# Kernel optimization log

Hardware: AMD Instinct MI355X
Metric: run time of the kernel (lower is better)

The kernel has to match this reference:

```python
import jax, jax.numpy as jnp
import numpy as np

P = 512        # number of graph pairs
MAXN = 192     # max(len_s) by construction
D_IN = 32      # num_input_features
HID = 64       # hidden_dim
REG = 0.1      # entropic reg
ITERS = 8      # numItermax in forward call
DEG = 8        # avg degree for synthetic edges


def setup_inputs() -> dict:
    key = jax.random.key(0)
    ks = jax.random.split(key, 16)
    len_s = np.asarray(96 + (np.arange(P) % 97), dtype=np.int32)          # 96..192
    len_t = np.asarray(32 + ((np.arange(P) * 7) % 65), dtype=np.int32)    # 32..96 <= len_s
    Ns, Nt = int(len_s.sum()), int(len_t.sum())
    return {
        "x_s": jax.random.normal(ks[0], (Ns, D_IN), jnp.float32),
        "x_t": jax.random.normal(ks[1], (Nt, D_IN), jnp.float32),
        "W_rel0": 0.1 * jax.random.normal(ks[2], (D_IN, HID), jnp.float32),
        "b_rel0": 0.1 * jax.random.normal(ks[3], (HID,), jnp.float32),
        "W_root0": 0.1 * jax.random.normal(ks[4], (D_IN, HID), jnp.float32),
        "W_rel1": 0.1 * jax.random.normal(ks[5], (HID, HID), jnp.float32),
        "b_rel1": 0.1 * jax.random.normal(ks[6], (HID,), jnp.float32),
        "W_root1": 0.1 * jax.random.normal(ks[7], (HID, HID), jnp.float32),
        "W_e": 0.1 * jax.random.normal(ks[8], (D_IN + 2 * HID, 64), jnp.float32),
        "b_e": 0.1 * jax.random.normal(ks[9], (64,), jnp.float32),
        "virtual": jax.random.uniform(ks[10], (64,), jnp.float32),
        "edge_index_s": jax.random.randint(ks[11], (2, Ns * DEG), 0, Ns, dtype=jnp.int32),
        "edge_index_t": jax.random.randint(ks[12], (2, Nt * DEG), 0, Nt, dtype=jnp.int32),
        "len_s": jnp.asarray(len_s),
        "len_t": jnp.asarray(len_t),
    }


def _normalize(x):
    return x / jnp.clip(jnp.linalg.norm(x, axis=-1, keepdims=True), 1e-12)


def _gnn_embed(x, ei, layers, W_e, b_e):
    # GraphConv: out = lin_rel(sum_{j->i} x_j) + lin_root(x_i), then relu; cat all layer outputs
    outs = [x]
    h = x
    for (Wr, br, Wo) in layers:
        agg = jax.ops.segment_sum(h[ei[0]], ei[1], num_segments=h.shape[0])
        h = jax.nn.relu(agg @ Wr + br + h @ Wo)
        outs.append(h)
    emb = jnp.concatenate(outs, axis=1) @ W_e + b_e
    return _normalize(emb)


def _pad_gather(emb, lens):
    # [total, E] -> [P, MAXN, E] via per-pair offsets (indices clipped; invalid masked later)
    off = jnp.cumsum(lens) - lens
    idx = jnp.clip(off[:, None] + jnp.arange(MAXN)[None, :], 0, emb.shape[0] - 1)
    return emb[idx]


def reference(x_s, x_t, W_rel0, b_rel0, W_root0, W_rel1, b_rel1, W_root1,
              W_e, b_e, virtual, edge_index_s, edge_index_t, len_s, len_t):
    layers = [(W_rel0, b_rel0, W_root0), (W_rel1, b_rel1, W_root1)]
    emb_s = _gnn_embed(x_s, edge_index_s, layers, W_e, b_e)  # [Ns, 64]
    emb_t = _gnn_embed(x_t, edge_index_t, layers, W_e, b_e)  # [Nt, 64]
    virt = _normalize(virtual[None, :])[0]

    s_pad = _pad_gather(emb_s, len_s)  # [P, MAXN, 64]
    t_pad = _pad_gather(emb_t, len_t)  # [P, MAXN, 64]
    j = jnp.arange(MAXN)
    # columns >= len_t use the virtual node embedding (covers j in [m, n))
    t_mask = (j[None, :] < len_t[:, None])[:, :, None]
    t_aug = jnp.where(t_mask, t_pad, virt[None, None, :])

    # Euclidean cdist via quadratic expansion
    sq_s = jnp.sum(s_pad * s_pad, -1)                              # [P, MAXN]
    sq_t = jnp.sum(t_aug * t_aug, -1)                              # [P, MAXN]
    dot = jnp.einsum('pid,pjd->pij', s_pad, t_aug)                 # [P, MAXN, MAXN]
    cd = jnp.sqrt(jnp.maximum(sq_s[:, :, None] + sq_t[:, None, :] - 2.0 * dot, 1e-12))

    # padded cost: real block = cdist, bottom-right pad block = 0, rest = 1000
    row_valid = j[None, :] < len_s[:, None]                        # [P, MAXN] (n = len_s)
    in_block = row_valid[:, :, None] & row_valid[:, None, :]
    pad_block = (~row_valid)[:, :, None] & (~row_valid)[:, None, :]
    cost = jnp.where(in_block, cd, jnp.where(pad_block, 0.0, 1000.0))

    # Sinkhorn-Knopp, a = b = ones(MAXN) so Kp = K and updates are 1/(K v), 1/(K^T u)
    K = jnp.exp(-cost / REG)

    def body(_, uv):
        u, v = uv
        v = 1.0 / jnp.einsum('pij,pi->pj', K, u)
        u = 1.0 / jnp.einsum('pij,pj->pi', K, v)
        return (u, v)

    u0 = jnp.full((P, MAXN), 1.0 / MAXN, dtype=cost.dtype)
    u, v = jax.lax.fori_loop(0, ITERS, body, (u0, u0))
    gamma = jax.lax.stop_gradient(u[:, :, None] * K * v[:, None, :])

    geds = jnp.sum(gamma * cost, axis=(1, 2))
    geds2 = geds / (len_s + len_t).astype(cost.dtype)
    return gamma, cost, geds2
```

## Files before the change

kernel.cpp:

```cpp
#include <hip/hip_runtime.h>
#include <math.h>

#define PAIRS 512
#define MAXN 192

#define LDS_BAR() asm volatile("s_waitcnt lgkmcnt(0)\n\ts_barrier" ::: "memory")

__global__ void offsets_kernel(const int* __restrict__ ls, const int* __restrict__ lt,
                               int* __restrict__ off) {
    __shared__ int wa[8], wb[8];
    int t = threadIdx.x;
    int a = ls[t], b = lt[t];
    int ia = a, ib = b;
#pragma unroll
    for (int d = 1; d < 64; d <<= 1) {
        int xa = __shfl_up(ia, d, 64);
        int xb = __shfl_up(ib, d, 64);
        if ((t & 63) >= d) { ia += xa; ib += xb; }
    }
    if ((t & 63) == 63) { wa[t >> 6] = ia; wb[t >> 6] = ib; }
    __syncthreads();
    int pa = 0, pb = 0;
    for (int w = 0; w < (t >> 6); w++) { pa += wa[w]; pb += wb[w]; }
    off[t] = pa + ia - a;
    off[PAIRS + t] = pb + ib - b;
}

__global__ __launch_bounds__(256) void count2_kernel(const int* __restrict__ eiS,
                                                     const int* __restrict__ eiT,
                                                     int* __restrict__ cnt,
                                                     int Es, int Et, int split) {
    int e = blockIdx.x * 256 + threadIdx.x;
    if (e < Es) atomicAdd(&cnt[eiS[Es + e]], 1);
    else if (e < Es + Et) atomicAdd(&cnt[split + eiT[Et + (e - Es)]], 1);
}

__global__ __launch_bounds__(256) void scan1_kernel(int* __restrict__ data,
                                                    int* __restrict__ blockSums, int N) {
    __shared__ int sc[256];
    int t = threadIdx.x;
    int base = blockIdx.x * 1024;
    int v[4];
    int s = 0;
#pragma unroll
    for (int q = 0; q < 4; q++) {
        int i = base + t * 4 + q;
        v[q] = (i < N) ? data[i] : 0;
        s += v[q];
    }
    sc[t] = s;
    __syncthreads();
    for (int d = 1; d < 256; d <<= 1) {
        int x = (t >= d) ? sc[t - d] : 0;
        __syncthreads();
        sc[t] += x;
        __syncthreads();
    }
    int excl = sc[t] - s;
#pragma unroll
    for (int q = 0; q < 4; q++) {
        int i = base + t * 4 + q;
        if (i < N) { data[i] = excl; excl += v[q]; }
    }
    if (t == 255) blockSums[blockIdx.x] = sc[255];
}

__global__ void scan2_kernel(int* __restrict__ blockSums, int B) {
    __shared__ int sh[256];
    int t = threadIdx.x;
    int v = (t < B) ? blockSums[t] : 0;
    sh[t] = v;
    __syncthreads();
    for (int d = 1; d < 256; d <<= 1) {
        int x = (t >= d) ? sh[t - d] : 0;
        __syncthreads();
        sh[t] += x;
        __syncthreads();
    }
    if (t < B) blockSums[t] = sh[t] - v;
}

__global__ __launch_bounds__(256) void scan3_kernel(int* __restrict__ data,
                                                    const int* __restrict__ blockSums,
                                                    int* __restrict__ cursor, int N) {
    int i = blockIdx.x * 256 + threadIdx.x;
    if (i < N) {
        int v = data[i] + blockSums[i >> 10];
        data[i] = v;
        cursor[i] = v;
    }
}

__global__ __launch_bounds__(256) void fill2_kernel(const int* __restrict__ eiS,
                                                    const int* __restrict__ eiT,
                                                    int* __restrict__ cursor,
                                                    int* __restrict__ src,
                                                    int Es, int Et, int split) {
    int e = blockIdx.x * 256 + threadIdx.x;
    if (e < Es) {
        int p = atomicAdd(&cursor[eiS[Es + e]], 1);
        src[p] = eiS[e];
    } else if (e < Es + Et) {
        int ee = e - Es;
        int p = atomicAdd(&cursor[split + eiT[Et + ee]], 1);
        src[p] = eiT[ee];
    }
}

template <int F>
__global__ __launch_bounds__(256) void gather_kernel(const float* __restrict__ featA,
                                                     const float* __restrict__ featB,
                                                     int split,
                                                     const int* __restrict__ rs,
                                                     const int* __restrict__ re,
                                                     const int* __restrict__ src,
                                                     float* __restrict__ agg, int N) {
    int gid = blockIdx.x * 256 + threadIdx.x;
    int row = gid / F;
    int lane = threadIdx.x & (F - 1);
    if (row >= N) return;
    int b = rs[row], e = re[row];
    int cnt = e - b;
    const float* feat = (row < split) ? featA : featB;
    int pre = cnt < F ? cnt : F;
    int sidx = (lane < cnt) ? src[b + lane] : 0;
    float acc = 0.f;
    for (int q = 0; q < pre; q++) {
        int s = __shfl(sidx, q, F);
        acc += feat[(size_t)s * F + lane];
    }
    for (int q = b + F; q < e; q++) acc += feat[(size_t)src[q] * F + lane];
    agg[(size_t)row * F + lane] = acc;
}


template <int KIN>
__global__ __launch_bounds__(256) void lin_gemm_kernel(const float* __restrict__ agg,
    const float* __restrict__ hinA, const float* __restrict__ hinB, int split,
    const float* __restrict__ Wrel, const float* __restrict__ brel,
    const float* __restrict__ Wroot, float* __restrict__ hout, int N) {
    __shared__ float Abuf[64 * 65];
    __shared__ float4 Wbuf[64 * 16];
    int tid = threadIdx.x;
    int i = tid & 15, j = tid >> 4;
    int rowbase = blockIdx.x * 64;
    float4 bv = ((const float4*)brel)[j];
    float acc[4][4];
#pragma unroll
    for (int r = 0; r < 4; r++) { acc[r][0] = bv.x; acc[r][1] = bv.y; acc[r][2] = bv.z; acc[r][3] = bv.w; }

    for (int c0 = 0; c0 < 2 * KIN; c0 += 64) {
        __syncthreads();
        for (int t = tid; t < 1024; t += 256) {
            int r = t >> 4, k4 = t & 15;
            int kg = c0 + 4 * k4;
            int row = rowbase + r; if (row >= N) row = N - 1;
            float4 v;
            if (kg < KIN) {
                v = ((const float4*)(agg + (size_t)row * KIN))[kg >> 2];
            } else {
                int kk = kg - KIN;
                const float* h = (row < split) ? hinA + (size_t)row * KIN
                                               : hinB + (size_t)(row - split) * KIN;
                v = ((const float4*)h)[kk >> 2];
            }
            float* d = Abuf + r * 65 + 4 * k4;
            d[0] = v.x; d[1] = v.y; d[2] = v.z; d[3] = v.w;
        }
        for (int t = tid; t < 1024; t += 256) {
            int k = t >> 4, jj = t & 15;
            int kg = c0 + k;
            const float* Wsrc = (kg < KIN) ? (Wrel + (size_t)kg * 64)
                                           : (Wroot + (size_t)(kg - KIN) * 64);
            Wbuf[t] = ((const float4*)Wsrc)[jj];
        }
        __syncthreads();
#pragma unroll 4
        for (int k = 0; k < 64; k++) {
            float4 wv = Wbuf[k * 16 + j];
            float a0 = Abuf[(4 * i + 0) * 65 + k];
            float a1 = Abuf[(4 * i + 1) * 65 + k];
            float a2 = Abuf[(4 * i + 2) * 65 + k];
            float a3 = Abuf[(4 * i + 3) * 65 + k];
            acc[0][0] = fmaf(a0, wv.x, acc[0][0]); acc[0][1] = fmaf(a0, wv.y, acc[0][1]);
            acc[0][2] = fmaf(a0, wv.z, acc[0][2]); acc[0][3] = fmaf(a0, wv.w, acc[0][3]);
            acc[1][0] = fmaf(a1, wv.x, acc[1][0]); acc[1][1] = fmaf(a1, wv.y, acc[1][1]);
            acc[1][2] = fmaf(a1, wv.z, acc[1][2]); acc[1][3] = fmaf(a1, wv.w, acc[1][3]);
            acc[2][0] = fmaf(a2, wv.x, acc[2][0]); acc[2][1] = fmaf(a2, wv.y, acc[2][1]);
            acc[2][2] = fmaf(a2, wv.z, acc[2][2]); acc[2][3] = fmaf(a2, wv.w, acc[2][3]);
            acc[3][0] = fmaf(a3, wv.x, acc[3][0]); acc[3][1] = fmaf(a3, wv.y, acc[3][1]);
            acc[3][2] = fmaf(a3, wv.z, acc[3][2]); acc[3][3] = fmaf(a3, wv.w, acc[3][3]);
        }
    }
#pragma unroll
    for (int r = 0; r < 4; r++) {
        int row = rowbase + 4 * i + r;
        if (row < N) {
            float4 o = make_float4(fmaxf(acc[r][0], 0.f), fmaxf(acc[r][1], 0.f),
                                   fmaxf(acc[r][2], 0.f), fmaxf(acc[r][3], 0.f));
            ((float4*)(hout + (size_t)row * 64))[j] = o;
        }
    }
}

__global__ __launch_bounds__(256) void lin64_emb_kernel(
    const float* __restrict__ agg, const float* __restrict__ h1,
    const float* __restrict__ xA, const float* __restrict__ xB, int split,
    const float* __restrict__ Wrel, const float* __restrict__ brel,
    const float* __restrict__ Wroot,
    const float* __restrict__ We, const float* __restrict__ be,
    float* __restrict__ emb, int N) {
    __shared__ float Abuf[64 * 65];
    __shared__ float4 Wbuf[64 * 16];
    __shared__ float h2buf[64 * 68];
    int tid = threadIdx.x;
    int i = tid & 15, j = tid >> 4;
    int rowbase = blockIdx.x * 64;

    {
        float4 bv = ((const float4*)brel)[j];
        float acc[4][4];
#pragma unroll
        for (int r = 0; r < 4; r++) { acc[r][0] = bv.x; acc[r][1] = bv.y; acc[r][2] = bv.z; acc[r][3] = bv.w; }

        for (int c0 = 0; c0 < 128; c0 += 64) {
            __syncthreads();
            for (int t = tid; t < 1024; t += 256) {
                int r = t >> 4, k4 = t & 15;
                int kg = c0 + 4 * k4;
                int row = rowbase + r; if (row >= N) row = N - 1;
                float4 v;
                if (kg < 64) v = ((const float4*)(agg + (size_t)row * 64))[kg >> 2];
                else         v = ((const float4*)(h1 + (size_t)row * 64))[(kg - 64) >> 2];
                float* d = Abuf + r * 65 + 4 * k4;
                d[0] = v.x; d[1] = v.y; d[2] = v.z; d[3] = v.w;
            }
            for (int t = tid; t < 1024; t += 256) {
                int k = t >> 4, jj = t & 15;
                int kg = c0 + k;
                const float* Wsrc = (kg < 64) ? (Wrel + (size_t)kg * 64)
                                              : (Wroot + (size_t)(kg - 64) * 64);
                Wbuf[t] = ((const float4*)Wsrc)[jj];
            }
            __syncthreads();
#pragma unroll 4
            for (int k = 0; k < 64; k++) {
                float4 wv = Wbuf[k * 16 + j];
                float a0 = Abuf[(4 * i + 0) * 65 + k];
                float a1 = Abuf[(4 * i + 1) * 65 + k];
                float a2 = Abuf[(4 * i + 2) * 65 + k];
                float a3 = Abuf[(4 * i + 3) * 65 + k];
                acc[0][0] = fmaf(a0, wv.x, acc[0][0]); acc[0][1] = fmaf(a0, wv.y, acc[0][1]);
                acc[0][2] = fmaf(a0, wv.z, acc[0][2]); acc[0][3] = fmaf(a0, wv.w, acc[0][3]);
                acc[1][0] = fmaf(a1, wv.x, acc[1][0]); acc[1][1] = fmaf(a1, wv.y, acc[1][1]);
                acc[1][2] = fmaf(a1, wv.z, acc[1][2]); acc[1][3] = fmaf(a1, wv.w, acc[1][3]);
                acc[2][0] = fmaf(a2, wv.x, acc[2][0]); acc[2][1] = fmaf(a2, wv.y, acc[2][1]);
                acc[2][2] = fmaf(a2, wv.z, acc[2][2]); acc[2][3] = fmaf(a2, wv.w, acc[2][3]);
                acc[3][0] = fmaf(a3, wv.x, acc[3][0]); acc[3][1] = fmaf(a3, wv.y, acc[3][1]);
                acc[3][2] = fmaf(a3, wv.z, acc[3][2]); acc[3][3] = fmaf(a3, wv.w, acc[3][3]);
            }
        }
#pragma unroll
        for (int r = 0; r < 4; r++) {
            float* d = h2buf + (4 * i + r) * 68 + 4 * j;
            d[0] = fmaxf(acc[r][0], 0.f); d[1] = fmaxf(acc[r][1], 0.f);
            d[2] = fmaxf(acc[r][2], 0.f); d[3] = fmaxf(acc[r][3], 0.f);
        }
    }

    float4 bv = ((const float4*)be)[j];
    float acc[4][4];
#pragma unroll
    for (int r = 0; r < 4; r++) { acc[r][0] = bv.x; acc[r][1] = bv.y; acc[r][2] = bv.z; acc[r][3] = bv.w; }

    for (int c0 = 0; c0 < 96; c0 += 64) {
        int kw = (96 - c0 < 64) ? 32 : 64;
        int sh = (kw == 64) ? 4 : 3;
        int msk = (1 << sh) - 1;
        __syncthreads();
        for (int t = tid; t < 64 * (kw >> 2); t += 256) {
            int r = t >> sh, k4 = t & msk;
            int kg = c0 + 4 * k4;
            int row = rowbase + r; if (row >= N) row = N - 1;
            float4 v;
            if (kg < 32) {
                const float* x = (row < split) ? xA + (size_t)row * 32
                                               : xB + (size_t)(row - split) * 32;
                v = ((const float4*)x)[kg >> 2];
            } else {
                v = ((const float4*)(h1 + (size_t)row * 64))[(kg - 32) >> 2];
            }
            float* d = Abuf + r * 65 + 4 * k4;
            d[0] = v.x; d[1] = v.y; d[2] = v.z; d[3] = v.w;
        }
        for (int t = tid; t < kw * 16; t += 256) {
            int k = t >> 4, jj = t & 15;
            Wbuf[t] = ((const float4*)(We + (size_t)(c0 + k) * 64))[jj];
        }
        __syncthreads();
#pragma unroll 4
        for (int k = 0; k < kw; k++) {
            float4 wv = Wbuf[k * 16 + j];
            float a0 = Abuf[(4 * i + 0) * 65 + k];
            float a1 = Abuf[(4 * i + 1) * 65 + k];
            float a2 = Abuf[(4 * i + 2) * 65 + k];
            float a3 = Abuf[(4 * i + 3) * 65 + k];
            acc[0][0] = fmaf(a0, wv.x, acc[0][0]); acc[0][1] = fmaf(a0, wv.y, acc[0][1]);
            acc[0][2] = fmaf(a0, wv.z, acc[0][2]); acc[0][3] = fmaf(a0, wv.w, acc[0][3]);
            acc[1][0] = fmaf(a1, wv.x, acc[1][0]); acc[1][1] = fmaf(a1, wv.y, acc[1][1]);
            acc[1][2] = fmaf(a1, wv.z, acc[1][2]); acc[1][3] = fmaf(a1, wv.w, acc[1][3]);
            acc[2][0] = fmaf(a2, wv.x, acc[2][0]); acc[2][1] = fmaf(a2, wv.y, acc[2][1]);
            acc[2][2] = fmaf(a2, wv.z, acc[2][2]); acc[2][3] = fmaf(a2, wv.w, acc[2][3]);
            acc[3][0] = fmaf(a3, wv.x, acc[3][0]); acc[3][1] = fmaf(a3, wv.y, acc[3][1]);
            acc[3][2] = fmaf(a3, wv.z, acc[3][2]); acc[3][3] = fmaf(a3, wv.w, acc[3][3]);
        }
    }
    __syncthreads();
    for (int t = tid; t < 1024; t += 256) {
        int k = t >> 4, jj = t & 15;
        Wbuf[t] = ((const float4*)(We + (size_t)(96 + k) * 64))[jj];
    }
    __syncthreads();
#pragma unroll 4
    for (int k = 0; k < 64; k++) {
        float4 wv = Wbuf[k * 16 + j];
        float a0 = h2buf[(4 * i + 0) * 68 + k];
        float a1 = h2buf[(4 * i + 1) * 68 + k];
        float a2 = h2buf[(4 * i + 2) * 68 + k];
        float a3 = h2buf[(4 * i + 3) * 68 + k];
        acc[0][0] = fmaf(a0, wv.x, acc[0][0]); acc[0][1] = fmaf(a0, wv.y, acc[0][1]);
        acc[0][2] = fmaf(a0, wv.z, acc[0][2]); acc[0][3] = fmaf(a0, wv.w, acc[0][3]);
        acc[1][0] = fmaf(a1, wv.x, acc[1][0]); acc[1][1] = fmaf(a1, wv.y, acc[1][1]);
        acc[1][2] = fmaf(a1, wv.z, acc[1][2]); acc[1][3] = fmaf(a1, wv.w, acc[1][3]);
        acc[2][0] = fmaf(a2, wv.x, acc[2][0]); acc[2][1] = fmaf(a2, wv.y, acc[2][1]);
        acc[2][2] = fmaf(a2, wv.z, acc[2][2]); acc[2][3] = fmaf(a2, wv.w, acc[2][3]);
        acc[3][0] = fmaf(a3, wv.x, acc[3][0]); acc[3][1] = fmaf(a3, wv.y, acc[3][1]);
        acc[3][2] = fmaf(a3, wv.z, acc[3][2]); acc[3][3] = fmaf(a3, wv.w, acc[3][3]);
    }
    __syncthreads();
#pragma unroll
    for (int r = 0; r < 4; r++)
#pragma unroll
        for (int c = 0; c < 4; c++)
            Abuf[(4 * i + r) * 65 + 4 * j + c] = acc[r][c];
    __syncthreads();
    int lane = tid & 63, wv = tid >> 6;
    for (int rr = 0; rr < 16; rr++) {
        int r = wv * 16 + rr;
        float val = Abuf[r * 65 + lane];
        float ss = val * val;
#pragma unroll
        for (int d = 32; d > 0; d >>= 1) ss += __shfl_xor(ss, d, 64);
        int row = rowbase + r;
        if (row < N) emb[(size_t)row * 64 + lane] = val / fmaxf(sqrtf(ss), 1e-12f);
    }
}

__device__ __forceinline__ void dot_half(float kh[3][12], const float* sS, const float* sT,
                                         int ti, int tj) {
#pragma unroll
    for (int s = 0; s < 3; s++)
#pragma unroll
        for (int b = 0; b < 12; b++) kh[s][b] = 0.f;
    for (int k4 = 0; k4 < 16; k4++) {
        float4 a0 = *(const float4*)(sS + (3 * ti + 0) * 68 + 4 * k4);
        float4 a1 = *(const float4*)(sS + (3 * ti + 1) * 68 + 4 * k4);
        float4 a2 = *(const float4*)(sS + (3 * ti + 2) * 68 + 4 * k4);
#pragma unroll
        for (int b = 0; b < 12; b++) {
            float4 tb = *(const float4*)(sT + (12 * tj + b) * 68 + 4 * k4);
            kh[0][b] = fmaf(a0.x, tb.x, kh[0][b]);
            kh[0][b] = fmaf(a0.y, tb.y, kh[0][b]);
            kh[0][b] = fmaf(a0.z, tb.z, kh[0][b]);
            kh[0][b] = fmaf(a0.w, tb.w, kh[0][b]);
            kh[1][b] = fmaf(a1.x, tb.x, kh[1][b]);
            kh[1][b] = fmaf(a1.y, tb.y, kh[1][b]);
            kh[1][b] = fmaf(a1.z, tb.z, kh[1][b]);
            kh[1][b] = fmaf(a1.w, tb.w, kh[1][b]);
            kh[2][b] = fmaf(a2.x, tb.x, kh[2][b]);
            kh[2][b] = fmaf(a2.y, tb.y, kh[2][b]);
            kh[2][b] = fmaf(a2.z, tb.z, kh[2][b]);
            kh[2][b] = fmaf(a2.w, tb.w, kh[2][b]);
        }
    }
}

__device__ __forceinline__ void epi_half(float kh[3][12], const float* sqS, const float* sqT,
                                         int h, int ti, int tj, int n, int p,
                                         float* __restrict__ cost_out) {
#pragma unroll
    for (int s = 0; s < 3; s++) {
        int i = 96 * h + 3 * ti + s;
        bool rv = i < n;
        float sqi = sqS[3 * ti + s];
        float tmp[12];
#pragma unroll
        for (int b = 0; b < 12; b++) {
            int j = 12 * tj + b;
            float cd = sqrtf(fmaxf(sqi + sqT[j] - 2.f * kh[s][b], 1e-12f));
            float c = (rv && (j < n)) ? cd : ((!rv && (j >= n)) ? 0.f : 1000.f);
            tmp[b] = c;
            kh[s][b] = __expf(-10.f * c);
        }
        float* orow = cost_out + ((size_t)p * MAXN + i) * MAXN + 12 * tj;
#pragma unroll
        for (int q = 0; q < 3; q++)
            ((float4*)orow)[q] = make_float4(tmp[4 * q], tmp[4 * q + 1],
                                             tmp[4 * q + 2], tmp[4 * q + 3]);
    }
}

__global__ __launch_bounds__(512, 4) void fused_cost_sinkhorn_kernel(
    const float* __restrict__ embS, const float* __restrict__ embT,
    const float* __restrict__ vraw,
    const int* __restrict__ lenS, const int* __restrict__ lenT,
    const int* __restrict__ off,
    float* __restrict__ cost_out, float* __restrict__ gamma_out,
    float* __restrict__ geds2, int Ns) {
    __shared__ __align__(16) float sT[192 * 68];
    __shared__ __align__(16) float sS[96 * 68];
    __shared__ __align__(16) float sqT[192];
    __shared__ __align__(16) float sqS[96];
    __shared__ __align__(16) float virtv[64];

    int p = blockIdx.x;
    int tid = threadIdx.x;
    int ti = tid & 31;
    int tj = tid >> 5;
    int n = lenS[p], m = lenT[p];
    int offs = off[p], offt = off[PAIRS + p];

    if (tid < 64) {
        float v = vraw[tid];
        float ss = v * v;
#pragma unroll
        for (int d = 32; d > 0; d >>= 1) ss += __shfl_xor(ss, d, 64);
        virtv[tid] = v / fmaxf(sqrtf(ss), 1e-12f);
    }
    __syncthreads();

    for (int t = tid; t < 192 * 16; t += 512) {
        int j = t >> 4, q = t & 15;
        float4 vv = (j < m) ? ((const float4*)embT)[(size_t)(offt + j) * 16 + q]
                            : ((const float4*)virtv)[q];
        *(float4*)(sT + j * 68 + 4 * q) = vv;
    }
    for (int t = tid; t < 96 * 16; t += 512) {
        int r = t >> 4, q = t & 15;
        int gi = offs + r; if (gi > Ns - 1) gi = Ns - 1;
        float4 vv = ((const float4*)embS)[(size_t)gi * 16 + q];
        *(float4*)(sS + r * 68 + 4 * q) = vv;
    }
    __syncthreads();
    if (tid < 192) {
        float s = 0.f;
#pragma unroll
        for (int k = 0; k < 64; k++) { float a = sT[tid * 68 + k]; s = fmaf(a, a, s); }
        sqT[tid] = s;
    } else if (tid < 288) {
        int r = tid - 192;
        float s = 0.f;
#pragma unroll
        for (int k = 0; k < 64; k++) { float a = sS[r * 68 + k]; s = fmaf(a, a, s); }
        sqS[r] = s;
    }
    __syncthreads();

    float kf[2][3][12];

    dot_half(kf[0], sS, sT, ti, tj);
    float4 pf0, pf1, pf2;
    {
        int t0 = tid, t1 = tid + 512, t2 = tid + 1024;
        int gi0 = offs + 96 + (t0 >> 4); if (gi0 > Ns - 1) gi0 = Ns - 1;
        int gi1 = offs + 96 + (t1 >> 4); if (gi1 > Ns - 1) gi1 = Ns - 1;
        int gi2 = offs + 96 + (t2 >> 4); if (gi2 > Ns - 1) gi2 = Ns - 1;
        pf0 = ((const float4*)embS)[(size_t)gi0 * 16 + (t0 & 15)];
        pf1 = ((const float4*)embS)[(size_t)gi1 * 16 + (t1 & 15)];
        pf2 = ((const float4*)embS)[(size_t)gi2 * 16 + (t2 & 15)];
    }
    epi_half(kf[0], sqS, sqT, 0, ti, tj, n, p, cost_out);

    LDS_BAR();
    {
        int t0 = tid, t1 = tid + 512, t2 = tid + 1024;
        *(float4*)(sS + (t0 >> 4) * 68 + 4 * (t0 & 15)) = pf0;
        *(float4*)(sS + (t1 >> 4) * 68 + 4 * (t1 & 15)) = pf1;
        *(float4*)(sS + (t2 >> 4) * 68 + 4 * (t2 & 15)) = pf2;
    }
    LDS_BAR();
    if (tid < 96) {
        float s = 0.f;
#pragma unroll
        for (int k = 0; k < 64; k++) { float a = sS[tid * 68 + k]; s = fmaf(a, a, s); }
        sqS[tid] = s;
    }
    LDS_BAR();

    dot_half(kf[1], sS, sT, ti, tj);
    epi_half(kf[1], sqS, sqT, 1, ti, tj, n, p, cost_out);
    LDS_BAR();

    float* part = sS;
    float* ubuf = sS + 6336;
    float* vbuf = sqT;

    if (tid < 192) ubuf[tid] = 1.f / 192.f;
    LDS_BAR();

    for (int it = 0; it < 8; it++) {
        float uloc[6];
#pragma unroll
        for (int h = 0; h < 2; h++)
#pragma unroll
            for (int s = 0; s < 3; s++) uloc[3 * h + s] = ubuf[96 * h + 3 * ti + s];
#pragma unroll
        for (int b = 0; b < 12; b++) {
            float a = 0.f;
#pragma unroll
            for (int h = 0; h < 2; h++)
#pragma unroll
                for (int s = 0; s < 3; s++) a = fmaf(kf[h][s][b], uloc[3 * h + s], a);
            part[(12 * tj + b) * 33 + ti] = a;
        }
        LDS_BAR();
        if (tid < 192) {
            float s = 0.f;
#pragma unroll
            for (int g = 0; g < 32; g++) s += part[tid * 33 + g];
            vbuf[tid] = 1.f / s;
        }
        LDS_BAR();
        float vloc[12];
        {
            float4 va = *(const float4*)(vbuf + 12 * tj);
            float4 vb = *(const float4*)(vbuf + 12 * tj + 4);
            float4 vc = *(const float4*)(vbuf + 12 * tj + 8);
            vloc[0] = va.x; vloc[1] = va.y; vloc[2] = va.z; vloc[3] = va.w;
            vloc[4] = vb.x; vloc[5] = vb.y; vloc[6] = vb.z; vloc[7] = vb.w;
            vloc[8] = vc.x; vloc[9] = vc.y; vloc[10] = vc.z; vloc[11] = vc.w;
        }
#pragma unroll
        for (int h = 0; h < 2; h++)
#pragma unroll
            for (int s = 0; s < 3; s++) {
                float a = 0.f;
#pragma unroll
                for (int b = 0; b < 12; b++) a = fmaf(kf[h][s][b], vloc[b], a);
                part[tj * 192 + 96 * h + 3 * ti + s] = a;
            }
        LDS_BAR();
        if (tid < 192) {
            float s = 0.f;
#pragma unroll
            for (int g = 0; g < 16; g++) s += part[g * 192 + tid];
            ubuf[tid] = 1.f / s;
        }
        LDS_BAR();
    }

    float vloc[12];
    {
        float4 va = *(const float4*)(vbuf + 12 * tj);
        float4 vb = *(const float4*)(vbuf + 12 * tj + 4);
        float4 vc = *(const float4*)(vbuf + 12 * tj + 8);
        vloc[0] = va.x; vloc[1] = va.y; vloc[2] = va.z; vloc[3] = va.w;
        vloc[4] = vb.x; vloc[5] = vb.y; vloc[6] = vb.z; vloc[7] = vb.w;
        vloc[8] = vc.x; vloc[9] = vc.y; vloc[10] = vc.z; vloc[11] = vc.w;
    }
    float accg = 0.f;
#pragma unroll
    for (int h = 0; h < 2; h++)
#pragma unroll
        for (int s = 0; s < 3; s++) {
            int i = 96 * h + 3 * ti + s;
            float ui = ubuf[i];
            float tmp[12];
#pragma unroll
            for (int b = 0; b < 12; b++) {
                float Kij = kf[h][s][b];
                float gg = ui * Kij * vloc[b];
                tmp[b] = gg;
                if (Kij > 0.f) accg = fmaf(gg, -0.1f * __logf(Kij), accg);
            }
            float* grow = gamma_out + ((size_t)p * MAXN + i) * MAXN + 12 * tj;
#pragma unroll
            for (int q = 0; q < 3; q++)
                ((float4*)grow)[q] = make_float4(tmp[4 * q], tmp[4 * q + 1],
                                                 tmp[4 * q + 2], tmp[4 * q + 3]);
        }
#pragma unroll
    for (int d = 32; d > 0; d >>= 1) accg += __shfl_xor(accg, d, 64);
    if ((tid & 63) == 0) sqS[tid >> 6] = accg;
    LDS_BAR();
    if (tid == 0) {
        float s = 0.f;
        for (int w = 0; w < 8; w++) s += sqS[w];
        geds2[p] = s / (float)(n + m);
    }
}

extern "C" void kernel_launch(void* const* d_in, const int* in_sizes, int n_in,
                              void* d_out, int out_size, void* d_ws, size_t ws_size,
                              hipStream_t stream) {
    const float* x_s     = (const float*)d_in[0];
    const float* x_t     = (const float*)d_in[1];
    const float* W_rel0  = (const float*)d_in[2];
    const float* b_rel0  = (const float*)d_in[3];
    const float* W_root0 = (const float*)d_in[4];
    const float* W_rel1  = (const float*)d_in[5];
    const float* b_rel1  = (const float*)d_in[6];
    const float* W_root1 = (const float*)d_in[7];
    const float* W_e     = (const float*)d_in[8];
    const float* b_e     = (const float*)d_in[9];
    const float* virt    = (const float*)d_in[10];
    const int*   ei_s    = (const int*)d_in[11];
    const int*   ei_t    = (const int*)d_in[12];
    const int*   len_s   = (const int*)d_in[13];
    const int*   len_t   = (const int*)d_in[14];

    int Ns = in_sizes[0] / 32;
    int Nt = in_sizes[1] / 32;
    int Es = in_sizes[11] / 2;
    int Et = in_sizes[12] / 2;
    int Ntot = Ns + Nt;
    int Etot = Es + Et;

    char* w = (char*)d_ws;
    int* off  = (int*)w;              w += 1024 * 4;
    int* bsum = (int*)w;              w += 256 * 4;
    int* rs   = (int*)w;              w += (size_t)Ntot * 4;
    int* cur  = (int*)w;              w += (size_t)Ntot * 4;
    int* src  = (int*)w;              w += (size_t)Etot * 4;
    w = (char*)(((size_t)w + 255) & ~(size_t)255);
    float* agg = (float*)w;           w += (size_t)Ntot * 64 * 4;
    float* h1  = (float*)w;           w += (size_t)Ntot * 64 * 4;

    float* out_gamma = (float*)d_out;
    float* out_cost  = out_gamma + (size_t)PAIRS * MAXN * MAXN;
    float* out_geds  = out_cost + (size_t)PAIRS * MAXN * MAXN;

    offsets_kernel<<<1, PAIRS, 0, stream>>>(len_s, len_t, off);

    hipMemsetAsync(rs, 0, (size_t)Ntot * 4, stream);
    count2_kernel<<<(Etot + 255) / 256, 256, 0, stream>>>(ei_s, ei_t, rs, Es, Et, Ns);
    int nb = (Ntot + 1023) / 1024;
    scan1_kernel<<<nb, 256, 0, stream>>>(rs, bsum, Ntot);
    scan2_kernel<<<1, 256, 0, stream>>>(bsum, nb);
    scan3_kernel<<<(Ntot + 255) / 256, 256, 0, stream>>>(rs, bsum, cur, Ntot);
    fill2_kernel<<<(Etot + 255) / 256, 256, 0, stream>>>(ei_s, ei_t, cur, src, Es, Et, Ns);

    int gblk = (Ntot + 63) / 64;

    gather_kernel<32><<<(int)(((long long)Ntot * 32 + 255) / 256), 256, 0, stream>>>(
        x_s, x_t, Ns, rs, cur, src, agg, Ntot);
    lin_gemm_kernel<32><<<gblk, 256, 0, stream>>>(
        agg, x_s, x_t, Ns, W_rel0, b_rel0, W_root0, h1, Ntot);
    gather_kernel<64><<<(int)(((long long)Ntot * 64 + 255) / 256), 256, 0, stream>>>(
        h1, h1, Ns, rs, cur, src, agg, Ntot);
    lin64_emb_kernel<<<gblk, 256, 0, stream>>>(
        agg, h1, x_s, x_t, Ns, W_rel1, b_rel1, W_root1, W_e, b_e, agg, Ntot);

    fused_cost_sinkhorn_kernel<<<PAIRS, 512, 0, stream>>>(
        agg, agg + (size_t)Ns * 64, virt, len_s, len_t, off,
        out_cost, out_gamma, out_geds, Ns);
}
```

Before: 559.1 us.

## Use 8x4 register tiles with transposed k-major LDS layout in GNN GEMMs

The two node-feature GEMM kernels now run with 128 threads, each computing an 8x4 output tile instead of 4x4. The A tile is stored transposed (k-major, stride 68) so each thread reads its eight rows as two float4 LDS loads per k step, rather than four scalar loads. The embedding GEMM is split into aligned 64/32/64 chunks over x, h1 and h2 with a shared inner macro. This raises arithmetic per LDS access but halves the threads per block and adds register pressure, with a transposing scatter on the LDS store side.

```diff
diff --git a/kernel.cpp b/kernel.cpp
--- a/kernel.cpp
+++ b/kernel.cpp
@@ -134,25 +134,39 @@
 }
 
 
+#define GEMM_INNER(KW, AKP, WBP)                                              \
+    _Pragma("unroll 4") for (int k = 0; k < (KW); k++) {                      \
+        float4 alo = *(const float4*)((AKP) + k * 68 + 8 * ig);               \
+        float4 ahi = *(const float4*)((AKP) + k * 68 + 8 * ig + 4);           \
+        float4 wv = (WBP)[k * 16 + jg];                                       \
+        float av[8] = {alo.x, alo.y, alo.z, alo.w, ahi.x, ahi.y, ahi.z, ahi.w}; \
+        _Pragma("unroll") for (int r = 0; r < 8; r++) {                       \
+            acc[r][0] = fmaf(av[r], wv.x, acc[r][0]);                         \
+            acc[r][1] = fmaf(av[r], wv.y, acc[r][1]);                         \
+            acc[r][2] = fmaf(av[r], wv.z, acc[r][2]);                         \
+            acc[r][3] = fmaf(av[r], wv.w, acc[r][3]);                         \
+        }                                                                     \
+    }
+
 template <int KIN>
-__global__ __launch_bounds__(256) void lin_gemm_kernel(const float* __restrict__ agg,
+__global__ __launch_bounds__(128) void lin_gemm_kernel(const float* __restrict__ agg,
     const float* __restrict__ hinA, const float* __restrict__ hinB, int split,
     const float* __restrict__ Wrel, const float* __restrict__ brel,
     const float* __restrict__ Wroot, float* __restrict__ hout, int N) {
-    __shared__ float Abuf[64 * 65];
-    __shared__ float4 Wbuf[64 * 16];
+    __shared__ float Ak[64 * 68];
+    __shared__ float4 Wb[64 * 16];
     int tid = threadIdx.x;
-    int i = tid & 15, j = tid >> 4;
+    int jg = tid & 15, ig = tid >> 4;
     int rowbase = blockIdx.x * 64;
-    float4 bv = ((const float4*)brel)[j];
-    float acc[4][4];
-#pragma unroll
-    for (int r = 0; r < 4; r++) { acc[r][0] = bv.x; acc[r][1] = bv.y; acc[r][2] = bv.z; acc[r][3] = bv.w; }
+    float4 bv = ((const float4*)brel)[jg];
+    float acc[8][4];
+#pragma unroll
+    for (int r = 0; r < 8; r++) { acc[r][0] = bv.x; acc[r][1] = bv.y; acc[r][2] = bv.z; acc[r][3] = bv.w; }
 
     for (int c0 = 0; c0 < 2 * KIN; c0 += 64) {
         __syncthreads();
-        for (int t = tid; t < 1024; t += 256) {
-            int r = t >> 4, k4 = t & 15;
+        for (int t = tid; t < 1024; t += 128) {
+            int k4 = t & 15, r = t >> 4;
             int kg = c0 + 4 * k4;
             int row = rowbase + r; if (row >= N) row = N - 1;
             float4 v;
@@ -164,190 +178,141 @@
                                                : hinB + (size_t)(row - split) * KIN;
                 v = ((const float4*)h)[kk >> 2];
             }
-            float* d = Abuf + r * 65 + 4 * k4;
-            d[0] = v.x; d[1] = v.y; d[2] = v.z; d[3] = v.w;
-        }
-        for (int t = tid; t < 1024; t += 256) {
+            float* d = Ak + (4 * k4) * 68 + r;
+            d[0] = v.x; d[68] = v.y; d[136] = v.z; d[204] = v.w;
+        }
+        for (int t = tid; t < 1024; t += 128) {
             int k = t >> 4, jj = t & 15;
             int kg = c0 + k;
             const float* Wsrc = (kg < KIN) ? (Wrel + (size_t)kg * 64)
                                            : (Wroot + (size_t)(kg - KIN) * 64);
-            Wbuf[t] = ((const float4*)Wsrc)[jj];
+            Wb[t] = ((const float4*)Wsrc)[jj];
         }
         __syncthreads();
-#pragma unroll 4
-        for (int k = 0; k < 64; k++) {
-            float4 wv = Wbuf[k * 16 + j];
-            float a0 = Abuf[(4 * i + 0) * 65 + k];
-            float a1 = Abuf[(4 * i + 1) * 65 + k];
-            float a2 = Abuf[(4 * i + 2) * 65 + k];
-            float a3 = Abuf[(4 * i + 3) * 65 + k];
-            acc[0][0] = fmaf(a0, wv.x, acc[0][0]); acc[0][1] = fmaf(a0, wv.y, acc[0][1]);
-            acc[0][2] = fmaf(a0, wv.z, acc[0][2]); acc[0][3] = fmaf(a0, wv.w, acc[0][3]);
-            acc[1][0] = fmaf(a1, wv.x, acc[1][0]); acc[1][1] = fmaf(a1, wv.y, acc[1][1]);
-            acc[1][2] = fmaf(a1, wv.z, acc[1][2]); acc[1][3] = fmaf(a1, wv.w, acc[1][3]);
-            acc[2][0] = fmaf(a2, wv.x, acc[2][0]); acc[2][1] = fmaf(a2, wv.y, acc[2][1]);
-            acc[2][2] = fmaf(a2, wv.z, acc[2][2]); acc[2][3] = fmaf(a2, wv.w, acc[2][3]);
-            acc[3][0] = fmaf(a3, wv.x, acc[3][0]); acc[3][1] = fmaf(a3, wv.y, acc[3][1]);
-            acc[3][2] = fmaf(a3, wv.z, acc[3][2]); acc[3][3] = fmaf(a3, wv.w, acc[3][3]);
-        }
-    }
-#pragma unroll
-    for (int r = 0; r < 4; r++) {
-        int row = rowbase + 4 * i + r;
+        GEMM_INNER(64, Ak, Wb)
+    }
+#pragma unroll
+    for (int r = 0; r < 8; r++) {
+        int row = rowbase + 8 * ig + r;
         if (row < N) {
             float4 o = make_float4(fmaxf(acc[r][0], 0.f), fmaxf(acc[r][1], 0.f),
                                    fmaxf(acc[r][2], 0.f), fmaxf(acc[r][3], 0.f));
-            ((float4*)(hout + (size_t)row * 64))[j] = o;
-        }
-    }
-}
-
-__global__ __launch_bounds__(256) void lin64_emb_kernel(
+            ((float4*)(hout + (size_t)row * 64))[jg] = o;
+        }
+    }
+}
+
+__global__ __launch_bounds__(128) void lin64_emb_kernel(
     const float* __restrict__ agg, const float* __restrict__ h1,
     const float* __restrict__ xA, const float* __restrict__ xB, int split,
     const float* __restrict__ Wrel, const float* __restrict__ brel,
     const float* __restrict__ Wroot,
     const float* __restrict__ We, const float* __restrict__ be,
     float* __restrict__ emb, int N) {
-    __shared__ float Abuf[64 * 65];
-    __shared__ float4 Wbuf[64 * 16];
+    __shared__ float Ak[64 * 68];
+    __shared__ float4 Wb[64 * 16];
     __shared__ float h2buf[64 * 68];
     int tid = threadIdx.x;
-    int i = tid & 15, j = tid >> 4;
+    int jg = tid & 15, ig = tid >> 4;
     int rowbase = blockIdx.x * 64;
 
     {
-        float4 bv = ((const float4*)brel)[j];
-        float acc[4][4];
-#pragma unroll
-        for (int r = 0; r < 4; r++) { acc[r][0] = bv.x; acc[r][1] = bv.y; acc[r][2] = bv.z; acc[r][3] = bv.w; }
+        float4 bv = ((const float4*)brel)[jg];
+        float acc[8][4];
+#pragma unroll
+        for (int r = 0; r < 8; r++) { acc[r][0] = bv.x; acc[r][1] = bv.y; acc[r][2] = bv.z; acc[r][3] = bv.w; }
 
         for (int c0 = 0; c0 < 128; c0 += 64) {
             __syncthreads();
-            for (int t = tid; t < 1024; t += 256) {
-                int r = t >> 4, k4 = t & 15;
+            for (int t = tid; t < 1024; t += 128) {
+                int k4 = t & 15, r = t >> 4;
                 int kg = c0 + 4 * k4;
                 int row = rowbase + r; if (row >= N) row = N - 1;
                 float4 v;
                 if (kg < 64) v = ((const float4*)(agg + (size_t)row * 64))[kg >> 2];
                 else         v = ((const float4*)(h1 + (size_t)row * 64))[(kg - 64) >> 2];
-                float* d = Abuf + r * 65 + 4 * k4;
-                d[0] = v.x; d[1] = v.y; d[2] = v.z; d[3] = v.w;
+                float* d = Ak + (4 * k4) * 68 + r;
+                d[0] = v.x; d[68] = v.y; d[136] = v.z; d[204] = v.w;
             }
-            for (int t = tid; t < 1024; t += 256) {
+            for (int t = tid; t < 1024; t += 128) {
                 int k = t >> 4, jj = t & 15;
                 int kg = c0 + k;
                 const float* Wsrc = (kg < 64) ? (Wrel + (size_t)kg * 64)
                                               : (Wroot + (size_t)(kg - 64) * 64);
-                Wbuf[t] = ((const float4*)Wsrc)[jj];
+                Wb[t] = ((const float4*)Wsrc)[jj];
             }
             __syncthreads();
-#pragma unroll 4
-            for (int k = 0; k < 64; k++) {
-                float4 wv = Wbuf[k * 16 + j];
-                float a0 = Abuf[(4 * i + 0) * 65 + k];
-                float a1 = Abuf[(4 * i + 1) * 65 + k];
-                float a2 = Abuf[(4 * i + 2) * 65 + k];
-                float a3 = Abuf[(4 * i + 3) * 65 + k];
-                acc[0][0] = fmaf(a0, wv.x, acc[0][0]); acc[0][1] = fmaf(a0, wv.y, acc[0][1]);
-                acc[0][2] = fmaf(a0, wv.z, acc[0][2]); acc[0][3] = fmaf(a0, wv.w, acc[0][3]);
-                acc[1][0] = fmaf(a1, wv.x, acc[1][0]); acc[1][1] = fmaf(a1, wv.y, acc[1][1]);
-                acc[1][2] = fmaf(a1, wv.z, acc[1][2]); acc[1][3] = fmaf(a1, wv.w, acc[1][3]);
-                acc[2][0] = fmaf(a2, wv.x, acc[2][0]); acc[2][1] = fmaf(a2, wv.y, acc[2][1]);
-                acc[2][2] = fmaf(a2, wv.z, acc[2][2]); acc[2][3] = fmaf(a2, wv.w, acc[2][3]);
-                acc[3][0] = fmaf(a3, wv.x, acc[3][0]); acc[3][1] = fmaf(a3, wv.y, acc[3][1]);
-                acc[3][2] = fmaf(a3, wv.z, acc[3][2]); acc[3][3] = fmaf(a3, wv.w, acc[3][3]);
-            }
-        }
-#pragma unroll
-        for (int r = 0; r < 4; r++) {
-            float* d = h2buf + (4 * i + r) * 68 + 4 * j;
-            d[0] = fmaxf(acc[r][0], 0.f); d[1] = fmaxf(acc[r][1], 0.f);
-            d[2] = fmaxf(acc[r][2], 0.f); d[3] = fmaxf(acc[r][3], 0.f);
-        }
-    }
-
-    float4 bv = ((const float4*)be)[j];
-    float acc[4][4];
-#pragma unroll
-    for (int r = 0; r < 4; r++) { acc[r][0] = bv.x; acc[r][1] = bv.y; acc[r][2] = bv.z; acc[r][3] = bv.w; }
-
-    for (int c0 = 0; c0 < 96; c0 += 64) {
-        int kw = (96 - c0 < 64) ? 32 : 64;
-        int sh = (kw == 64) ? 4 : 3;
-        int msk = (1 << sh) - 1;
-        __syncthreads();
-        for (int t = tid; t < 64 * (kw >> 2); t += 256) {
-            int r = t >> sh, k4 = t & msk;
-            int kg = c0 + 4 * k4;
-            int row = rowbase + r; if (row >= N) row = N - 1;
-            float4 v;
-            if (kg < 32) {
-                const float* x = (row < split) ? xA + (size_t)row * 32
-                                               : xB + (size_t)(row - split) * 32;
-                v = ((const float4*)x)[kg >> 2];
-            } else {
-                v = ((const float4*)(h1 + (size_t)row * 64))[(kg - 32) >> 2];
-            }
-            float* d = Abuf + r * 65 + 4 * k4;
-            d[0] = v.x; d[1] = v.y; d[2] = v.z; d[3] = v.w;
-        }
-        for (int t = tid; t < kw * 16; t += 256) {
-            int k = t >> 4, jj = t & 15;
-            Wbuf[t] = ((const float4*)(We + (size_t)(c0 + k) * 64))[jj];
-        }
-        __syncthreads();
-#pragma unroll 4
-        for (int k = 0; k < kw; k++) {
-            float4 wv = Wbuf[k * 16 + j];
-            float a0 = Abuf[(4 * i + 0) * 65 + k];
-            float a1 = Abuf[(4 * i + 1) * 65 + k];
-            float a2 = Abuf[(4 * i + 2) * 65 + k];
-            float a3 = Abuf[(4 * i + 3) * 65 + k];
-            acc[0][0] = fmaf(a0, wv.x, acc[0][0]); acc[0][1] = fmaf(a0, wv.y, acc[0][1]);
-            acc[0][2] = fmaf(a0, wv.z, acc[0][2]); acc[0][3] = fmaf(a0, wv.w, acc[0][3]);
-            acc[1][0] = fmaf(a1, wv.x, acc[1][0]); acc[1][1] = fmaf(a1, wv.y, acc[1][1]);
-            acc[1][2] = fmaf(a1, wv.z, acc[1][2]); acc[1][3] = fmaf(a1, wv.w, acc[1][3]);
-            acc[2][0] = fmaf(a2, wv.x, acc[2][0]); acc[2][1] = fmaf(a2, wv.y, acc[2][1]);
-            acc[2][2] = fmaf(a2, wv.z, acc[2][2]); acc[2][3] = fmaf(a2, wv.w, acc[2][3]);
-            acc[3][0] = fmaf(a3, wv.x, acc[3][0]); acc[3][1] = fmaf(a3, wv.y, acc[3][1]);
-            acc[3][2] = fmaf(a3, wv.z, acc[3][2]); acc[3][3] = fmaf(a3, wv.w, acc[3][3]);
-        }
-    }
-    __syncthreads();
-    for (int t = tid; t < 1024; t += 256) {
+            GEMM_INNER(64, Ak, Wb)
+        }
+#pragma unroll
+        for (int r = 0; r < 8; r++)
+#pragma unroll
+            for (int c = 0; c < 4; c++)
+                h2buf[(4 * jg + c) * 68 + 8 * ig + r] = fmaxf(acc[r][c], 0.f);
+    }
+
+    float4 bv = ((const float4*)be)[jg];
+    float acc[8][4];
+#pragma unroll
+    for (int r = 0; r < 8; r++) { acc[r][0] = bv.x; acc[r][1] = bv.y; acc[r][2] = bv.z; acc[r][3] = bv.w; }
+
+    __syncthreads();
+    for (int t = tid; t < 1024; t += 128) {
+        int k4 = t & 15, r = t >> 4;
+        int kg = 4 * k4;
+        int row = rowbase + r; if (row >= N) row = N - 1;
+        float4 v;
+        if (kg < 32) {
+            const float* x = (row < split) ? xA + (size_t)row * 32
+                                           : xB + (size_t)(row - split) * 32;
+            v = ((const float4*)x)[kg >> 2];
+        } else {
+            v = ((const float4*)(h1 + (size_t)row * 64))[(kg - 32) >> 2];
+        }
+        float* d = Ak + (4 * k4) * 68 + r;
+        d[0] = v.x; d[68] = v.y; d[136] = v.z; d[204] = v.w;
+    }
+    for (int t = tid; t < 1024; t += 128) {
         int k = t >> 4, jj = t & 15;
-        Wbuf[t] = ((const float4*)(We + (size_t)(96 + k) * 64))[jj];
-    }
-    __syncthreads();
-#pragma unroll 4
-    for (int k = 0; k < 64; k++) {
-        float4 wv = Wbuf[k * 16 + j];
-        float a0 = h2buf[(4 * i + 0) * 68 + k];
-        float a1 = h2buf[(4 * i + 1) * 68 + k];
-        float a2 = h2buf[(4 * i + 2) * 68 + k];
-        float a3 = h2buf[(4 * i + 3) * 68 + k];
-        acc[0][0] = fmaf(a0, wv.x, acc[0][0]); acc[0][1] = fmaf(a0, wv.y, acc[0][1]);
-        acc[0][2] = fmaf(a0, wv.z, acc[0][2]); acc[0][3] = fmaf(a0, wv.w, acc[0][3]);
-        acc[1][0] = fmaf(a1, wv.x, acc[1][0]); acc[1][1] = fmaf(a1, wv.y, acc[1][1]);
-        acc[1][2] = fmaf(a1, wv.z, acc[1][2]); acc[1][3] = fmaf(a1, wv.w, acc[1][3]);
-        acc[2][0] = fmaf(a2, wv.x, acc[2][0]); acc[2][1] = fmaf(a2, wv.y, acc[2][1]);
-        acc[2][2] = fmaf(a2, wv.z, acc[2][2]); acc[2][3] = fmaf(a2, wv.w, acc[2][3]);
-        acc[3][0] = fmaf(a3, wv.x, acc[3][0]); acc[3][1] = fmaf(a3, wv.y, acc[3][1]);
-        acc[3][2] = fmaf(a3, wv.z, acc[3][2]); acc[3][3] = fmaf(a3, wv.w, acc[3][3]);
-    }
-    __syncthreads();
-#pragma unroll
-    for (int r = 0; r < 4; r++)
+        Wb[t] = ((const float4*)(We + (size_t)k * 64))[jj];
+    }
+    __syncthreads();
+    GEMM_INNER(64, Ak, Wb)
+
+    __syncthreads();
+    for (int t = tid; t < 512; t += 128) {
+        int k4 = t & 7, r = t >> 3;
+        int row = rowbase + r; if (row >= N) row = N - 1;
+        float4 v = ((const float4*)(h1 + (size_t)row * 64))[8 + k4];
+        float* d = Ak + (4 * k4) * 68 + r;
+        d[0] = v.x; d[68] = v.y; d[136] = v.z; d[204] = v.w;
+    }
+    for (int t = tid; t < 512; t += 128) {
+        int k = t >> 4, jj = t & 15;
+        Wb[t] = ((const float4*)(We + (size_t)(64 + k) * 64))[jj];
+    }
+    __syncthreads();
+    GEMM_INNER(32, Ak, Wb)
+
+    __syncthreads();
+    for (int t = tid; t < 1024; t += 128) {
+        int k = t >> 4, jj = t & 15;
+        Wb[t] = ((const float4*)(We + (size_t)(96 + k) * 64))[jj];
+    }
+    __syncthreads();
+    GEMM_INNER(64, h2buf, Wb)
+
+    __syncthreads();
+#pragma unroll
+    for (int r = 0; r < 8; r++)
 #pragma unroll
         for (int c = 0; c < 4; c++)
-            Abuf[(4 * i + r) * 65 + 4 * j + c] = acc[r][c];
+            Ak[(8 * ig + r) * 68 + 4 * jg + c] = acc[r][c];
     __syncthreads();
     int lane = tid & 63, wv = tid >> 6;
-    for (int rr = 0; rr < 16; rr++) {
-        int r = wv * 16 + rr;
-        float val = Abuf[r * 65 + lane];
+    for (int rr = 0; rr < 32; rr++) {
+        int r = wv * 32 + rr;
+        float val = Ak[r * 68 + lane];
         float ss = val * val;
 #pragma unroll
         for (int d = 32; d > 0; d >>= 1) ss += __shfl_xor(ss, d, 64);
@@ -654,11 +619,11 @@
 
     gather_kernel<32><<<(int)(((long long)Ntot * 32 + 255) / 256), 256, 0, stream>>>(
         x_s, x_t, Ns, rs, cur, src, agg, Ntot);
-    lin_gemm_kernel<32><<<gblk, 256, 0, stream>>>(
+    lin_gemm_kernel<32><<<gblk, 128, 0, stream>>>(
         agg, x_s, x_t, Ns, W_rel0, b_rel0, W_root0, h1, Ntot);
     gather_kernel<64><<<(int)(((long long)Ntot * 64 + 255) / 256), 256, 0, stream>>>(
         h1, h1, Ns, rs, cur, src, agg, Ntot);
-    lin64_emb_kernel<<<gblk, 256, 0, stream>>>(
+    lin64_emb_kernel<<<gblk, 128, 0, stream>>>(
         agg, h1, x_s, x_t, Ns, W_rel1, b_rel1, W_root1, W_e, b_e, agg, Ntot);
 
     fused_cost_sinkhorn_kernel<<<PAIRS, 512, 0, stream>>>(
```

Result: slower. 597.7 us (+6.9%).
